# Kernel optimization log

Hardware: AMD Instinct MI355X
Metric: run time of the kernel (lower is better)

The kernel has to match this reference:

```python
import jax, jax.numpy as jnp
import numpy as np

D = 768          # model dim (ViT-Base)
H = 12           # num heads
DH = 64          # head dim
DFF = 4 * D      # mlp hidden
SMAX = 1024      # max sequence length in the packed batch
LENS = np.array([1024, 896, 768, 640, 512, 448, 256, 64], dtype=np.int32)
TOTAL = int(LENS.sum())  # 4608
LN_EPS = 1e-6
NEG = -1e30


def _ln(x, w, b):
    mu = jnp.mean(x, axis=-1, keepdims=True)
    var = jnp.mean(jnp.square(x - mu), axis=-1, keepdims=True)
    return (x - mu) * jax.lax.rsqrt(var + LN_EPS) * w + b


def setup_inputs() -> dict:
    key = jax.random.key(0)
    ks = jax.random.split(key, 16)
    s = 0.02
    cu = jnp.asarray(np.concatenate([[0], np.cumsum(LENS)]).astype(np.int32))
    return {
        "x": jax.random.normal(ks[0], (TOTAL, D), jnp.float32),
        "norm1_w": jnp.ones((D,), jnp.float32),
        "norm1_b": jnp.zeros((D,), jnp.float32),
        "qkv_w": jax.random.normal(ks[1], (3 * D, D), jnp.float32) * s,
        "qkv_b": jnp.zeros((3 * D,), jnp.float32),
        "proj_w": jax.random.normal(ks[2], (D, D), jnp.float32) * s,
        "proj_b": jnp.zeros((D,), jnp.float32),
        "ls1_gamma": jax.random.normal(ks[3], (D,), jnp.float32) * 0.1,
        "norm2_w": jnp.ones((D,), jnp.float32),
        "norm2_b": jnp.zeros((D,), jnp.float32),
        "fc1_w": jax.random.normal(ks[4], (DFF, D), jnp.float32) * s,
        "fc1_b": jnp.zeros((DFF,), jnp.float32),
        "fc2_w": jax.random.normal(ks[5], (D, DFF), jnp.float32) * s,
        "fc2_b": jnp.zeros((D,), jnp.float32),
        "ls2_gamma": jax.random.normal(ks[6], (D,), jnp.float32) * 0.1,
        "cu_seqlens": cu,
    }


def reference(x, norm1_w, norm1_b, qkv_w, qkv_b, proj_w, proj_b, ls1_gamma,
              norm2_w, norm2_b, fc1_w, fc1_b, fc2_w, fc2_b, ls2_gamma,
              cu_seqlens):
    total = x.shape[0]
    B = cu_seqlens.shape[0] - 1
    tok = jnp.arange(total)
    seg = jnp.searchsorted(cu_seqlens[1:], tok, side="right")  # [Total]
    pos = tok - cu_seqlens[seg]                                 # [Total]
    lens = cu_seqlens[1:] - cu_seqlens[:-1]                     # [B]

    # --- attention branch ---
    xn = _ln(x, norm1_w, norm1_b)
    qkv = (xn @ qkv_w.T + qkv_b).reshape(total, 3, H, DH)
    q, k, v = qkv[:, 0], qkv[:, 1], qkv[:, 2]                   # [Total,H,DH]

    # pad packed ragged tokens to [B, SMAX, H, DH]
    def pad(t):
        return jnp.zeros((B, SMAX, H, DH), t.dtype).at[seg, pos].set(t)
    qp, kp, vp = pad(q), pad(k), pad(v)

    valid = jnp.arange(SMAX)[None, :] < lens[:, None]           # [B,SMAX]
    scores = jnp.einsum("bqhd,bkhd->bhqk", qp, kp) * (DH ** -0.5)
    scores = jnp.where(valid[:, None, None, :], scores, NEG)
    attn = jax.nn.softmax(scores, axis=-1)
    out = jnp.einsum("bhqk,bkhd->bqhd", attn, vp)
    out = out[seg, pos].reshape(total, D)                       # back to packed

    attn_out = out @ proj_w.T + proj_b
    x = x + ls1_gamma * attn_out

    # --- mlp branch ---
    xn2 = _ln(x, norm2_w, norm2_b)
    h = jax.nn.gelu(xn2 @ fc1_w.T + fc1_b, approximate=False)
    h = h @ fc2_w.T + fc2_b
    return x + ls2_gamma * h
```

## Files before the change

### kernel.cpp

```cpp
#include <hip/hip_runtime.h>
#include <hip/hip_bf16.h>
#include <stdint.h>

#define D 768
#define HEADS 12
#define DHEAD 64
#define DFF 3072
#define TOTAL 4608
#define NSEG 8

typedef __bf16 bf16;
typedef __bf16 bf16x8 __attribute__((ext_vector_type(8)));
typedef __bf16 bf16x4 __attribute__((ext_vector_type(4)));
typedef float f32x4 __attribute__((ext_vector_type(4)));

__device__ __forceinline__ void gld_lds16(const void* g, void* l) {
  __builtin_amdgcn_global_load_lds(
      (const __attribute__((address_space(1))) void*)g,
      (__attribute__((address_space(3))) void*)(uintptr_t)l, 16, 0, 0);
}

__global__ __launch_bounds__(256) void cvt_all_kernel(
    const float* __restrict__ a, const float* __restrict__ b,
    const float* __restrict__ c, const float* __restrict__ d,
    bf16* __restrict__ out, int nA, int nAB, int nABC, int nTot) {
  int i = blockIdx.x * blockDim.x + threadIdx.x;
  if (i >= nTot) return;
  const float* src;
  int j;
  if (i < nA) { src = a; j = i; }
  else if (i < nAB) { src = b; j = i - nA; }
  else if (i < nABC) { src = c; j = i - nAB; }
  else { src = d; j = i - nABC; }
  float4 v = ((const float4*)src)[j];
  bf16x4 o;
  o[0] = (bf16)v.x; o[1] = (bf16)v.y; o[2] = (bf16)v.z; o[3] = (bf16)v.w;
  ((bf16x4*)out)[i] = o;
}

__global__ __launch_bounds__(256) void ln_kernel(
    const float* __restrict__ x, const float* __restrict__ w,
    const float* __restrict__ b, bf16* __restrict__ out) {
  __shared__ float red[8];
  int row = blockIdx.x;
  const float* xr = x + (size_t)row * D;
  int t = threadIdx.x;
  float v[3];
  float s = 0.f, s2 = 0.f;
#pragma unroll
  for (int j = 0; j < 3; j++) {
    v[j] = xr[t + 256 * j];
    s += v[j]; s2 += v[j] * v[j];
  }
#pragma unroll
  for (int m = 1; m <= 32; m <<= 1) {
    s += __shfl_xor(s, m);
    s2 += __shfl_xor(s2, m);
  }
  int wave = t >> 6, lane = t & 63;
  if (lane == 0) { red[wave] = s; red[4 + wave] = s2; }
  __syncthreads();
  s = red[0] + red[1] + red[2] + red[3];
  s2 = red[4] + red[5] + red[6] + red[7];
  float mu = s * (1.f / 768.f);
  float var = s2 * (1.f / 768.f) - mu * mu;
  float rstd = rsqrtf(var + 1e-6f);
#pragma unroll
  for (int j = 0; j < 3; j++) {
    int c = t + 256 * j;
    out[(size_t)row * D + c] = (bf16)((v[j] - mu) * rstd * w[c] + b[c]);
  }
}

__device__ __forceinline__ float fast_gelu(float v) {
  float u = v * (0.7978845608f + 0.0356774081f * v * v);
  float e = exp2f(2.8853900818f * u);
  float th = 1.f - 2.f * __builtin_amdgcn_rcpf(1.f + e);
  return 0.5f * v * (1.f + th);
}

template <int MODE, int TN, int BK, int GX, int GY>
__global__ __launch_bounds__(256) void gemm_kernel(
    const bf16* __restrict__ A, const bf16* __restrict__ W,
    const float* __restrict__ bias, const float* __restrict__ res,
    const float* __restrict__ gamma, bf16* __restrict__ outb,
    float* __restrict__ outf, int N, int K) {
  constexpr int NJ = TN / 32;
  constexpr int KH = BK / 32;
  constexpr int CG = BK / 8;
  constexpr int SH = (BK == 32) ? 1 : 0;
  constexpr int LPR = BK / 8;
  constexpr int RS = 64 / LPR;
  constexpr int RB = TN / 4;
  __shared__ __align__(16) bf16 As[2][128 * BK];
  __shared__ __align__(16) bf16 Bs[2][TN * BK];

  const int g = blockIdx.x;
  const int xc = g & 7, q = g >> 3;
  const int bx = q % GX, by = xc + 8 * (q / GX);
  if (by >= GY) return;
  const int m0 = by * 128, n0 = bx * TN;

  const int t = threadIdx.x, wave = t >> 6, lane = t & 63;
  const int quad = lane >> 4, l16 = lane & 15;
  const int wm = (wave & 1) * 64, wn = (wave >> 1) * (TN / 2);

  const int ar = lane / LPR, ac = lane % LPR;
  const int acg = ac ^ (((wave * 32 + ar) >> SH) & (CG - 1));
  const int bcg = ac ^ (((wave * RB + ar) >> SH) & (CG - 1));
  const bf16* gA = A + (size_t)(m0 + wave * 32 + ar) * K + acg * 8;
  const bf16* gB = W + (size_t)(n0 + wave * RB + ar) * K + bcg * 8;

  auto stage = [&](int buf) {
#pragma unroll
    for (int n = 0; n < 32 / RS; n++)
      gld_lds16(gA + (size_t)n * RS * K, &As[buf][(wave * 32 + n * RS) * BK]);
#pragma unroll
    for (int n = 0; n < RB / RS; n++)
      gld_lds16(gB + (size_t)n * RS * K, &Bs[buf][(wave * RB + n * RS) * BK]);
    gA += BK; gB += BK;
  };

  stage(0);

  f32x4 acc[4][NJ] = {};
  int cur = 0;
  for (int k0 = 0; k0 < K; k0 += BK) {
    __syncthreads();
    if (k0 + BK < K) stage(cur ^ 1);
    const bf16* as = As[cur];
    const bf16* bs = Bs[cur];
    bf16x8 af[KH][4], bg[KH][NJ];
#pragma unroll
    for (int kh = 0; kh < KH; kh++) {
#pragma unroll
      for (int i = 0; i < 4; i++) {
        int R = wm + i * 16 + l16;
        af[kh][i] = *(const bf16x8*)&as[R * BK + 8 * ((kh * 4 + quad) ^ ((R >> SH) & (CG - 1)))];
      }
#pragma unroll
      for (int j = 0; j < NJ; j++) {
        int R = wn + j * 16 + l16;
        bg[kh][j] = *(const bf16x8*)&bs[R * BK + 8 * ((kh * 4 + quad) ^ ((R >> SH) & (CG - 1)))];
      }
    }
#pragma unroll
    for (int kh = 0; kh < KH; kh++)
#pragma unroll
      for (int i = 0; i < 4; i++)
#pragma unroll
        for (int j = 0; j < NJ; j++)
          acc[i][j] = __builtin_amdgcn_mfma_f32_16x16x32_bf16(af[kh][i], bg[kh][j], acc[i][j], 0, 0, 0);
    cur ^= 1;
  }

#pragma unroll
  for (int i = 0; i < 4; i++)
#pragma unroll
    for (int j = 0; j < NJ; j++)
#pragma unroll
      for (int r = 0; r < 4; r++) {
        int row = m0 + wm + i * 16 + quad * 4 + r;
        int col = n0 + wn + j * 16 + l16;
        float v = acc[i][j][r] + bias[col];
        if (MODE == 0) {
          outb[(size_t)row * N + col] = (bf16)v;
        } else if (MODE == 1) {
          outf[(size_t)row * N + col] = res[(size_t)row * N + col] + gamma[col] * v;
        } else {
          outb[(size_t)row * N + col] = (bf16)fast_gelu(v);
        }
      }
}

__global__ __launch_bounds__(256) void attn_kernel(
    const bf16* __restrict__ qkv, const int* __restrict__ cu,
    bf16* __restrict__ attn) {
  __shared__ __align__(16) bf16 Ks[64][72];
  __shared__ __align__(16) bf16 VTs[64][64];

  const int qt = blockIdx.x, h = blockIdx.y;
  const int tok0 = qt * 64;
  int b = 0;
  while (cu[b + 1] <= tok0) b++;
  const int s0 = cu[b], S = cu[b + 1] - s0;

  const int t = threadIdx.x, wave = t >> 6, lane = t & 63;
  const int quad = lane >> 4, l16 = lane & 15;

  const size_t qrow = (size_t)(tok0 + wave * 16 + l16) * (3 * D) + h * 64;
  const bf16x8 bq0 = *(const bf16x8*)&qkv[qrow + quad * 8];
  const bf16x8 bq1 = *(const bf16x8*)&qkv[qrow + 32 + quad * 8];

  const int srow = t >> 2, sc0 = (t & 3) * 16;
  const size_t kbase = (size_t)(s0 + srow) * (3 * D) + h * 64 + sc0 + D;
  const int vr0 = (t & 15) * 4, vd0 = (t >> 4) * 4;
  const size_t vbase = (size_t)(s0 + vr0) * (3 * D) + h * 64 + vd0 + 2 * D;
  const int kB0 = ((vr0 >> 5) << 5) | (((vr0 >> 2) & 3) << 3) | (((vr0 >> 4) & 1) << 2);

  bf16x8 kr0 = *(const bf16x8*)&qkv[kbase];
  bf16x8 kr1 = *(const bf16x8*)&qkv[kbase + 8];
  bf16x4 vp[4];
#pragma unroll
  for (int i = 0; i < 4; i++)
    vp[i] = *(const bf16x4*)&qkv[vbase + (size_t)i * (3 * D)];

  f32x4 Oacc[4] = {};
  float li = 0.f;
  const float SC = 0.125f * 1.44269504089f;

  for (int kb = 0; kb < S; kb += 64) {
    __syncthreads();
    *(bf16x8*)&Ks[srow][sc0] = kr0;
    *(bf16x8*)&Ks[srow][sc0 + 8] = kr1;
#pragma unroll
    for (int j = 0; j < 4; j++) {
      int d = vd0 + j;
      bf16x4 w;
      w[0] = vp[0][j]; w[1] = vp[1][j]; w[2] = vp[2][j]; w[3] = vp[3][j];
      *(bf16x4*)&VTs[d][kB0 ^ ((d & 7) * 8)] = w;
    }
    __syncthreads();

    if (kb + 64 < S) {
      const size_t koff = kbase + (size_t)(kb + 64) * (3 * D);
      const size_t voff = vbase + (size_t)(kb + 64) * (3 * D);
      kr0 = *(const bf16x8*)&qkv[koff];
      kr1 = *(const bf16x8*)&qkv[koff + 8];
#pragma unroll
      for (int i = 0; i < 4; i++)
        vp[i] = *(const bf16x4*)&qkv[voff + (size_t)i * (3 * D)];
    }

    f32x4 sac[4];
#pragma unroll
    for (int nt = 0; nt < 4; nt++) {
      bf16x8 ak0 = *(const bf16x8*)&Ks[nt * 16 + l16][quad * 8];
      bf16x8 ak1 = *(const bf16x8*)&Ks[nt * 16 + l16][32 + quad * 8];
      f32x4 z = {};
      z = __builtin_amdgcn_mfma_f32_16x16x32_bf16(ak0, bq0, z, 0, 0, 0);
      sac[nt] = __builtin_amdgcn_mfma_f32_16x16x32_bf16(ak1, bq1, z, 0, 0, 0);
    }

    bf16x8 bv0, bv1;
    float ls = 0.f;
#pragma unroll
    for (int r = 0; r < 4; r++) {
      float e0 = exp2f(sac[0][r] * SC);
      float e1 = exp2f(sac[1][r] * SC);
      float e2 = exp2f(sac[2][r] * SC);
      float e3 = exp2f(sac[3][r] * SC);
      ls += (e0 + e1) + (e2 + e3);
      bv0[r] = (bf16)e0; bv0[4 + r] = (bf16)e1;
      bv1[r] = (bf16)e2; bv1[4 + r] = (bf16)e3;
    }
    li += ls;

    const int vsw = (l16 & 7) * 8;
#pragma unroll
    for (int dt = 0; dt < 4; dt++) {
      bf16x8 av0 = *(const bf16x8*)&VTs[dt * 16 + l16][(quad * 8) ^ vsw];
      bf16x8 av1 = *(const bf16x8*)&VTs[dt * 16 + l16][(32 + quad * 8) ^ vsw];
      Oacc[dt] = __builtin_amdgcn_mfma_f32_16x16x32_bf16(av0, bv0, Oacc[dt], 0, 0, 0);
      Oacc[dt] = __builtin_amdgcn_mfma_f32_16x16x32_bf16(av1, bv1, Oacc[dt], 0, 0, 0);
    }
  }

  li += __shfl_xor(li, 16);
  li += __shfl_xor(li, 32);
  const float inv = 1.f / li;

  __syncthreads();
  bf16(*Osh)[72] = (bf16(*)[72])Ks;
  const int orow = wave * 16 + l16;
#pragma unroll
  for (int dt = 0; dt < 4; dt++) {
    int dg = dt * 16 + quad * 4;
    bf16x4 w;
#pragma unroll
    for (int r = 0; r < 4; r++) w[r] = (bf16)(Oacc[dt][r] * inv);
    *(bf16x4*)&Osh[orow][dg ^ ((l16 & 7) * 8)] = w;
  }
  const int osw = (l16 & 7) * 8;
  bf16x8 o0 = *(const bf16x8*)&Osh[orow][(quad * 16) ^ osw];
  bf16x8 o1 = *(const bf16x8*)&Osh[orow][(quad * 16 + 8) ^ osw];
  const size_t obase = (size_t)(tok0 + orow) * D + h * 64 + quad * 16;
  *(bf16x8*)&attn[obase] = o0;
  *(bf16x8*)&attn[obase + 8] = o1;
}

extern "C" void kernel_launch(void* const* d_in, const int* in_sizes, int n_in,
                              void* d_out, int out_size, void* d_ws,
                              size_t ws_size, hipStream_t stream) {
  const float* x       = (const float*)d_in[0];
  const float* norm1_w = (const float*)d_in[1];
  const float* norm1_b = (const float*)d_in[2];
  const float* qkv_w   = (const float*)d_in[3];
  const float* qkv_b   = (const float*)d_in[4];
  const float* proj_w  = (const float*)d_in[5];
  const float* proj_b  = (const float*)d_in[6];
  const float* ls1     = (const float*)d_in[7];
  const float* norm2_w = (const float*)d_in[8];
  const float* norm2_b = (const float*)d_in[9];
  const float* fc1_w   = (const float*)d_in[10];
  const float* fc1_b   = (const float*)d_in[11];
  const float* fc2_w   = (const float*)d_in[12];
  const float* fc2_b   = (const float*)d_in[13];
  const float* ls2     = (const float*)d_in[14];
  const int*   cu      = (const int*)d_in[15];
  float* out = (float*)d_out;

  char* ws = (char*)d_ws;
  size_t off = 0;
  auto alloc = [&](size_t bytes) {
    void* p = ws + off;
    off += (bytes + 255) & ~(size_t)255;
    return p;
  };
  bf16* w_qkv  = (bf16*)alloc((size_t)3 * D * D * 2);
  bf16* w_proj = (bf16*)alloc((size_t)D * D * 2);
  bf16* w_fc1  = (bf16*)alloc((size_t)DFF * D * 2);
  bf16* w_fc2  = (bf16*)alloc((size_t)D * DFF * 2);
  bf16* xn     = (bf16*)alloc((size_t)TOTAL * D * 2);
  bf16* qkv    = (bf16*)alloc((size_t)TOTAL * 3 * D * 2);
  bf16* attnb  = (bf16*)alloc((size_t)TOTAL * D * 2);
  float* x1    = (float*)alloc((size_t)TOTAL * D * 4);
  bf16* hbuf   = qkv;

  {
    int nA   = 3 * D * D / 4;
    int nAB  = nA + D * D / 4;
    int nABC = nAB + DFF * D / 4;
    int nTot = nABC + D * DFF / 4;
    cvt_all_kernel<<<(nTot + 255) / 256, 256, 0, stream>>>(
        qkv_w, proj_w, fc1_w, fc2_w, w_qkv, nA, nAB, nABC, nTot);
  }

  ln_kernel<<<TOTAL, 256, 0, stream>>>(x, norm1_w, norm1_b, xn);

  constexpr int GY = TOTAL / 128;
  constexpr int GYP = ((GY + 7) / 8) * 8;

  gemm_kernel<0, 128, 64, 18, GY><<<18 * GYP, 256, 0, stream>>>(
      xn, w_qkv, qkv_b, nullptr, nullptr, qkv, nullptr, 3 * D, D);

  dim3 ga(TOTAL / 64, HEADS);
  attn_kernel<<<ga, 256, 0, stream>>>(qkv, cu, attnb);

  gemm_kernel<1, 64, 64, 12, GY><<<12 * GYP, 256, 0, stream>>>(
      attnb, w_proj, proj_b, x, ls1, nullptr, x1, D, D);

  ln_kernel<<<TOTAL, 256, 0, stream>>>(x1, norm2_w, norm2_b, xn);

  gemm_kernel<2, 128, 64, 24, GY><<<24 * GYP, 256, 0, stream>>>(
      xn, w_fc1, fc1_b, nullptr, nullptr, hbuf, nullptr, DFF, D);

  gemm_kernel<1, 64, 64, 12, GY><<<12 * GYP, 256, 0, stream>>>(
      hbuf, w_fc2, fc2_b, x1, ls2, nullptr, out, D, DFF);
}
```

Measured before the change: 257.7 us.

## Double-buffer K/V tiles in attention and swap grid order to heads-first

The attention kernel moves from a single LDS buffer with two barriers per tile to two K/V LDS buffers. Each iteration writes the next tile into the other buffer while computing on the current one, so only one barrier per tile is needed and global loads run further ahead. The grid is also transposed so the 12 heads of the same query tile launch next to each other, which may improve L2 reuse of the packed qkv rows. The cost is double the LDS footprint, which may lower occupancy, and more registers held for prefetch.

```diff
diff --git a/kernel.cpp b/kernel.cpp
--- a/kernel.cpp
+++ b/kernel.cpp
@@ -176,14 +176,15 @@
 __global__ __launch_bounds__(256) void attn_kernel(
     const bf16* __restrict__ qkv, const int* __restrict__ cu,
     bf16* __restrict__ attn) {
-  __shared__ __align__(16) bf16 Ks[64][72];
-  __shared__ __align__(16) bf16 VTs[64][64];
-
-  const int qt = blockIdx.x, h = blockIdx.y;
+  __shared__ __align__(16) bf16 Ks[2][64][72];
+  __shared__ __align__(16) bf16 VTs[2][64][64];
+
+  const int qt = blockIdx.y, h = blockIdx.x;
   const int tok0 = qt * 64;
   int b = 0;
   while (cu[b + 1] <= tok0) b++;
   const int s0 = cu[b], S = cu[b + 1] - s0;
+  const int n = S >> 6;
 
   const int t = threadIdx.x, wave = t >> 6, lane = t & 63;
   const int quad = lane >> 4, l16 = lane & 15;
@@ -198,51 +199,44 @@
   const size_t vbase = (size_t)(s0 + vr0) * (3 * D) + h * 64 + vd0 + 2 * D;
   const int kB0 = ((vr0 >> 5) << 5) | (((vr0 >> 2) & 3) << 3) | (((vr0 >> 4) & 1) << 2);
 
-  bf16x8 kr0 = *(const bf16x8*)&qkv[kbase];
-  bf16x8 kr1 = *(const bf16x8*)&qkv[kbase + 8];
-  bf16x4 vp[4];
-#pragma unroll
-  for (int i = 0; i < 4; i++)
-    vp[i] = *(const bf16x4*)&qkv[vbase + (size_t)i * (3 * D)];
-
   f32x4 Oacc[4] = {};
   float li = 0.f;
   const float SC = 0.125f * 1.44269504089f;
 
-  for (int kb = 0; kb < S; kb += 64) {
-    __syncthreads();
-    *(bf16x8*)&Ks[srow][sc0] = kr0;
-    *(bf16x8*)&Ks[srow][sc0 + 8] = kr1;
+  bf16x8 kA0, kA1, kB0r, kB1r;
+  bf16x4 vA[4], vB[4];
+
+  auto loadT = [&](int tile, bf16x8& k0, bf16x8& k1, bf16x4* vp) {
+    const size_t ko = kbase + (size_t)tile * 64 * (3 * D);
+    const size_t vo = vbase + (size_t)tile * 64 * (3 * D);
+    k0 = *(const bf16x8*)&qkv[ko];
+    k1 = *(const bf16x8*)&qkv[ko + 8];
+#pragma unroll
+    for (int i = 0; i < 4; i++)
+      vp[i] = *(const bf16x4*)&qkv[vo + (size_t)i * (3 * D)];
+  };
+  auto writeT = [&](int buf, const bf16x8& k0, const bf16x8& k1, const bf16x4* vp) {
+    *(bf16x8*)&Ks[buf][srow][sc0] = k0;
+    *(bf16x8*)&Ks[buf][srow][sc0 + 8] = k1;
 #pragma unroll
     for (int j = 0; j < 4; j++) {
       int d = vd0 + j;
       bf16x4 w;
       w[0] = vp[0][j]; w[1] = vp[1][j]; w[2] = vp[2][j]; w[3] = vp[3][j];
-      *(bf16x4*)&VTs[d][kB0 ^ ((d & 7) * 8)] = w;
-    }
-    __syncthreads();
-
-    if (kb + 64 < S) {
-      const size_t koff = kbase + (size_t)(kb + 64) * (3 * D);
-      const size_t voff = vbase + (size_t)(kb + 64) * (3 * D);
-      kr0 = *(const bf16x8*)&qkv[koff];
-      kr1 = *(const bf16x8*)&qkv[koff + 8];
-#pragma unroll
-      for (int i = 0; i < 4; i++)
-        vp[i] = *(const bf16x4*)&qkv[voff + (size_t)i * (3 * D)];
-    }
-
+      *(bf16x4*)&VTs[buf][d][kB0 ^ ((d & 7) * 8)] = w;
+    }
+  };
+  auto computeT = [&](int buf) {
     f32x4 sac[4];
 #pragma unroll
     for (int nt = 0; nt < 4; nt++) {
-      bf16x8 ak0 = *(const bf16x8*)&Ks[nt * 16 + l16][quad * 8];
-      bf16x8 ak1 = *(const bf16x8*)&Ks[nt * 16 + l16][32 + quad * 8];
+      bf16x8 ak0 = *(const bf16x8*)&Ks[buf][nt * 16 + l16][quad * 8];
+      bf16x8 ak1 = *(const bf16x8*)&Ks[buf][nt * 16 + l16][32 + quad * 8];
       f32x4 z = {};
       z = __builtin_amdgcn_mfma_f32_16x16x32_bf16(ak0, bq0, z, 0, 0, 0);
       sac[nt] = __builtin_amdgcn_mfma_f32_16x16x32_bf16(ak1, bq1, z, 0, 0, 0);
     }
-
-    bf16x8 bv0, bv1;
+    bf16x8 pv0, pv1;
     float ls = 0.f;
 #pragma unroll
     for (int r = 0; r < 4; r++) {
@@ -251,19 +245,34 @@
       float e2 = exp2f(sac[2][r] * SC);
       float e3 = exp2f(sac[3][r] * SC);
       ls += (e0 + e1) + (e2 + e3);
-      bv0[r] = (bf16)e0; bv0[4 + r] = (bf16)e1;
-      bv1[r] = (bf16)e2; bv1[4 + r] = (bf16)e3;
+      pv0[r] = (bf16)e0; pv0[4 + r] = (bf16)e1;
+      pv1[r] = (bf16)e2; pv1[4 + r] = (bf16)e3;
     }
     li += ls;
-
     const int vsw = (l16 & 7) * 8;
 #pragma unroll
     for (int dt = 0; dt < 4; dt++) {
-      bf16x8 av0 = *(const bf16x8*)&VTs[dt * 16 + l16][(quad * 8) ^ vsw];
-      bf16x8 av1 = *(const bf16x8*)&VTs[dt * 16 + l16][(32 + quad * 8) ^ vsw];
-      Oacc[dt] = __builtin_amdgcn_mfma_f32_16x16x32_bf16(av0, bv0, Oacc[dt], 0, 0, 0);
-      Oacc[dt] = __builtin_amdgcn_mfma_f32_16x16x32_bf16(av1, bv1, Oacc[dt], 0, 0, 0);
-    }
+      bf16x8 av0 = *(const bf16x8*)&VTs[buf][dt * 16 + l16][(quad * 8) ^ vsw];
+      bf16x8 av1 = *(const bf16x8*)&VTs[buf][dt * 16 + l16][(32 + quad * 8) ^ vsw];
+      Oacc[dt] = __builtin_amdgcn_mfma_f32_16x16x32_bf16(av0, pv0, Oacc[dt], 0, 0, 0);
+      Oacc[dt] = __builtin_amdgcn_mfma_f32_16x16x32_bf16(av1, pv1, Oacc[dt], 0, 0, 0);
+    }
+  };
+
+  loadT(0, kA0, kA1, vA);
+  if (n > 1) loadT(1, kB0r, kB1r, vB);
+  writeT(0, kA0, kA1, vA);
+
+  for (int tt = 0; tt < n; tt += 2) {
+    __syncthreads();
+    if (tt + 1 < n) writeT(1, kB0r, kB1r, vB);
+    if (tt + 2 < n) loadT(tt + 2, kA0, kA1, vA);
+    computeT(0);
+    if (tt + 1 >= n) break;
+    __syncthreads();
+    if (tt + 2 < n) writeT(0, kA0, kA1, vA);
+    if (tt + 3 < n) loadT(tt + 3, kB0r, kB1r, vB);
+    computeT(1);
   }
 
   li += __shfl_xor(li, 16);
@@ -271,7 +280,7 @@
   const float inv = 1.f / li;
 
   __syncthreads();
-  bf16(*Osh)[72] = (bf16(*)[72])Ks;
+  bf16(*Osh)[72] = (bf16(*)[72])Ks[0];
   const int orow = wave * 16 + l16;
 #pragma unroll
   for (int dt = 0; dt < 4; dt++) {
@@ -344,7 +353,7 @@
   gemm_kernel<0, 128, 64, 18, GY><<<18 * GYP, 256, 0, stream>>>(
       xn, w_qkv, qkv_b, nullptr, nullptr, qkv, nullptr, 3 * D, D);
 
-  dim3 ga(TOTAL / 64, HEADS);
+  dim3 ga(HEADS, TOTAL / 64);
   attn_kernel<<<ga, 256, 0, stream>>>(qkv, cu, attnb);
 
   gemm_kernel<1, 64, 64, 12, GY><<<12 * GYP, 256, 0, stream>>>(
```

Result: no change. 261.8 us (+1.6%).
